# Optimization experiments

Hardware: AMD Instinct MI355X
Metric: run time of the kernel (lower is better)

## Reference

```python
import jax, jax.numpy as jnp
import numpy as np

ROPE_BASE = 10000.0
WINDOW = 1024  # per_layer_sliding_window
SCALE = 0.08838834764831845  # 1/sqrt(128)
NEG_INF = -1e30


def _apply_rope(x, positions):
    # x: [B, S, H, D]; positions: [B, S] int
    D = x.shape[-1]
    inv_freq = 1.0 / (ROPE_BASE ** (jnp.arange(0, D, 2, dtype=jnp.float32) / D))  # [D/2]
    ang = positions.astype(jnp.float32)[..., None] * inv_freq          # [B, S, D/2]
    cos = jnp.cos(ang)[:, :, None, :]                                   # [B, S, 1, D/2]
    sin = jnp.sin(ang)[:, :, None, :]
    x1, x2 = x[..., : D // 2], x[..., D // 2 :]
    return jnp.concatenate([x1 * cos - x2 * sin, x2 * cos + x1 * sin], axis=-1)


def setup_inputs() -> dict:
    key = jax.random.key(0)
    k1, k2, k3, k4 = jax.random.split(key, 4)
    B, S, H, KV, D = 1, 2048, 32, 8, 128
    q = jax.random.normal(k1, (B, S, H, D), dtype=jnp.float32)
    k = jax.random.normal(k2, (B, S, KV, D), dtype=jnp.float32)
    v = jax.random.normal(k3, (B, S, KV, D), dtype=jnp.float32)
    positions = jnp.broadcast_to(jnp.arange(S, dtype=jnp.int32), (B, S))
    sinks = jax.random.normal(k4, (H,), dtype=jnp.float32)
    return {"q": q, "k": k, "v": v, "positions": positions, "sinks": sinks}


def reference(q, k, v, positions, sinks):
    # q: [B,S,H,D]; k,v: [B,S,KV,D]; positions: [B,S]; sinks: [H]
    B, S, H, D = q.shape
    KV = k.shape[2]
    group = H // KV

    qr = _apply_rope(q, positions)
    kr = _apply_rope(k, positions)

    # GQA: expand kv heads to match q heads
    kr = jnp.repeat(kr, group, axis=2)  # [B,S,H,D]
    ve = jnp.repeat(v, group, axis=2)   # [B,S,H,D]

    scores = jnp.einsum("bqhd,bkhd->bhqk", qr, kr) * SCALE  # [B,H,Q,K]

    pq = positions[:, :, None]  # [B,Q,1]
    pk = positions[:, None, :]  # [B,1,K]
    allowed = (pk <= pq) & (pq - pk < WINDOW)               # causal + sliding window
    scores = jnp.where(allowed[:, None, :, :], scores, NEG_INF)

    # softmax with per-head attention sink logit in the denominator
    sink = sinks[None, :, None]                             # [1,H,1]
    m = jnp.maximum(jnp.max(scores, axis=-1), sink)         # [B,H,Q]
    p = jnp.exp(scores - m[..., None])                      # [B,H,Q,K]
    denom = jnp.sum(p, axis=-1) + jnp.exp(sink - m)         # [B,H,Q]
    out = jnp.einsum("bhqk,bkhd->bqhd", p, ve) / denom.transpose(0, 2, 1)[..., None]
    return out  # [B,S,H,D]
```

## Files before the change

### kernel.cpp

```cpp
#include <hip/hip_runtime.h>

#define S_LEN 2048
#define NH 32
#define NKV 8
#define HD 128
#define WINDOW 1024
#define NEG_INF_F -1e30f
#define NEG_L2_10K_O64 -0.2076205059304601f
#define LOG2E_F 1.442695040888963f

typedef unsigned short ushort_t;
typedef __attribute__((ext_vector_type(4))) short bf16x4;
typedef __attribute__((ext_vector_type(8))) short short8;
typedef __attribute__((ext_vector_type(2))) unsigned uint2v;
typedef __attribute__((ext_vector_type(4))) float floatx4;

static __device__ __forceinline__ float fexp2(float x) {
  return __builtin_amdgcn_exp2f(x);
}

static __device__ __forceinline__ ushort_t f2bf(float f) {
  union { float f; unsigned u; } un; un.f = f;
  unsigned r = un.u + 0x7fffu + ((un.u >> 16) & 1u);
  return (ushort_t)(r >> 16);
}

static __device__ __forceinline__ unsigned pack2bf(float a, float b) {
  return (unsigned)f2bf(a) | ((unsigned)f2bf(b) << 16);
}

static __device__ __forceinline__ unsigned packP(float a, float b) {
  unsigned ua = __builtin_bit_cast(unsigned, a) + 0x8000u;
  unsigned ub = __builtin_bit_cast(unsigned, b) + 0x8000u;
  return __builtin_amdgcn_perm(ub, ua, 0x07060302u);
}

__device__ __forceinline__ void gl_lds16(const ushort_t* g, ushort_t* l) {
  __builtin_amdgcn_global_load_lds(
      (const __attribute__((address_space(1))) unsigned int*)g,
      (__attribute__((address_space(3))) unsigned int*)l, 16, 0, 0);
}

__global__ __launch_bounds__(256) void prep_kv(
    const float* __restrict__ k, const float* __restrict__ v,
    const int* __restrict__ positions, ushort_t* __restrict__ Kr,
    ushort_t* __restrict__ Vt) {
  __shared__ float lv[64][129];
  const int kv = blockIdx.x & 7;
  const int s0 = (blockIdx.x >> 3) * 64;
  const int tid = threadIdx.x;
  {
    const int i = tid & 63;
    const int wrow = tid >> 6;
    const float invf = fexp2((float)i * NEG_L2_10K_O64);
#pragma unroll 4
    for (int it = 0; it < 16; ++it) {
      int s = s0 + it * 4 + wrow;
      float pos = (float)positions[s];
      const float* kp = k + ((size_t)s * NKV + kv) * HD;
      float x1 = kp[i], x2 = kp[i + 64];
      float sn, cs;
      __sincosf(pos * invf, &sn, &cs);
      ushort_t* o = Kr + ((size_t)kv * S_LEN + s) * HD;
      o[i] = f2bf(x1 * cs - x2 * sn);
      o[i + 64] = f2bf(x2 * cs + x1 * sn);
    }
  }
  {
    const int d = tid & 127;
    const int r2 = tid >> 7;
#pragma unroll
    for (int it = 0; it < 32; ++it) {
      int row = it * 2 + r2;
      lv[row][d] = v[((size_t)(s0 + row) * NKV + kv) * HD + d];
    }
  }
  __syncthreads();
  {
    unsigned* Vreg = (unsigned*)(Vt + ((size_t)(kv * 32 + (s0 >> 6)) * HD) * 64);
#pragma unroll
    for (int it = 0; it < 16; ++it) {
      int idx = it * 256 + tid;
      int d = idx >> 5, j = idx & 31;
      Vreg[idx] = pack2bf(lv[2 * j][d], lv[2 * j + 1][d]);
    }
  }
}

__global__ __launch_bounds__(256, 3) void attn_kernel(
    const float* __restrict__ q, const int* __restrict__ positions,
    const float* __restrict__ sinks, const ushort_t* __restrict__ Kr,
    const ushort_t* __restrict__ Vt, float* __restrict__ out) {
  __shared__ __align__(16) ushort_t smem[16384];
  __shared__ float lsx[64];

  const int tid = threadIdx.x;
  const int w = tid >> 6;
  const int lane = tid & 63;
  const int quad = lane >> 4;
  const int l16 = lane & 15;
  const int hp = w >> 1;
  const int kh = w & 1;
  const int kv = blockIdx.x & 7;
  const int bid = blockIdx.x >> 3;
  const int h0 = kv * 4 + hp * 2;
  const float QSCALE = (float)(0.08838834764831845 * 1.4426950408889634);

  const ushort_t* KrH = Kr + (size_t)kv * S_LEN * HD;
  const ushort_t* VtH = Vt + (size_t)kv * 32 * HD * 64;

  int tiles[2];
  int ntiles;
  if (bid < 64) { tiles[0] = bid + 64; tiles[1] = 0; ntiles = 1; }
  else          { tiles[0] = bid - 64; tiles[1] = 127 - bid; ntiles = 2; }

  int kgo0, kgo1, vgo0, vgo1;
  { int key = tid >> 4;          kgo0 = key * HD + (((tid & 15) ^ (key & 15)) * 8); }
  { int s2 = 256 + tid; int key = s2 >> 4;
                                 kgo1 = key * HD + (((s2 & 15) ^ (key & 15)) * 8); }
  { int n = tid;       vgo0 = (n >> 2) * 64 + (((n & 3) ^ ((n >> 4) & 3)) * 8); }
  { int n = 256 + tid; vgo1 = (n >> 2) * 64 + (((n & 3) ^ ((n >> 4) & 3)) * 8); }
  const int kdst0 = (tid & 192) * 8;
  const int kdst1 = (256 + (tid & 192)) * 8;
  const int vdst0 = 8192 + (tid & 192) * 8;
  const int vdst1 = 8192 + 2048 + (tid & 192) * 8;
  const int kb8 = kh * 2 + (quad >> 1);
  const int vrd = (l16 * 4 + (kb8 ^ (l16 >> 2))) * 8 + (quad & 1) * 4;

  auto stage = [&](int b, int koff) {
    const ushort_t* kb = KrH + (size_t)koff * HD;
    const ushort_t* vb = VtH + (size_t)(koff >> 6) * HD * 64 + (koff & 32);
    gl_lds16(kb + kgo0, smem + b * 4096 + kdst0);
    gl_lds16(kb + kgo1, smem + b * 4096 + kdst1);
    gl_lds16(vb + vgo0, smem + b * 4096 + vdst0);
    gl_lds16(vb + vgo1, smem + b * 4096 + vdst1);
  };

  for (int ti = 0; ti < ntiles; ++ti) {
    const int tile = tiles[ti];
    const int q0 = tile * 16;

    {
      const int hw = kv * 4 + w;
      ushort_t* Qsw = smem + w * 2048;
      const float invf = fexp2((float)lane * NEG_L2_10K_O64);
#pragma unroll 4
      for (int row = 0; row < 16; ++row) {
        float pos = (float)positions[q0 + row];
        const float* qp = q + ((size_t)(q0 + row) * NH + hw) * HD;
        float x1 = qp[lane], x2 = qp[lane + 64];
        float sn, cs;
        __sincosf(pos * invf, &sn, &cs);
        float o1 = (x1 * cs - x2 * sn) * QSCALE;
        float o2 = (x2 * cs + x1 * sn) * QSCALE;
        int c1_ = (lane >> 3) ^ row;
        int c2_ = ((lane >> 3) + 8) ^ row;
        Qsw[row * 128 + c1_ * 8 + (lane & 7)] = f2bf(o1);
        Qsw[row * 128 + c2_ * 8 + (lane & 7)] = f2bf(o2);
      }
    }
    __syncthreads();
    short8 qf0[4], qf1[4];
    {
      const ushort_t* Qr0 = smem + (hp * 2) * 2048;
      const ushort_t* Qr1 = smem + (hp * 2 + 1) * 2048;
#pragma unroll
      for (int t = 0; t < 4; ++t) {
        int off = l16 * 128 + (((4 * t + quad) ^ l16) * 8);
        qf0[t] = *(const short8*)&Qr0[off];
        qf1[t] = *(const short8*)&Qr1[off];
      }
    }
    __syncthreads();

    floatx4 OA[8], OB[8];
#pragma unroll
    for (int i = 0; i < 8; ++i) {
      OA[i] = (floatx4){0.f, 0.f, 0.f, 0.f};
      OB[i] = (floatx4){0.f, 0.f, 0.f, 0.f};
    }
    float lsumA = 0.f, lsumB = 0.f;

    const int cbeg = (q0 > 1023) ? ((q0 - 1023) >> 5) : 0;
    const int cend = (q0 + 15) >> 5;

    stage(0, cbeg * 32);
    __syncthreads();

    for (int ci = cbeg; ci <= cend; ++ci) {
      const int b = (ci - cbeg) & 1;
      const int koff = ci * 32;
      if (ci < cend) stage(b ^ 1, koff + 32);

      const ushort_t* KsB = smem + b * 4096 + (kh * 16) * 128;
      floatx4 sA = {0.f, 0.f, 0.f, 0.f}, sB = {0.f, 0.f, 0.f, 0.f};
#pragma unroll
      for (int t = 0; t < 4; ++t) {
        short8 kf = *(const short8*)&KsB[l16 * 128 + (((4 * t + quad) ^ l16) * 8)];
        sA = __builtin_amdgcn_mfma_f32_16x16x32_bf16(kf, qf0[t], sA, 0, 0, 0);
        sB = __builtin_amdgcn_mfma_f32_16x16x32_bf16(kf, qf1[t], sB, 0, 0, 0);
      }

      if (koff + 31 > q0 || koff < q0 - 1008) {
        const int qp_ = q0 + l16;
        const int kb_ = koff + kh * 16 + quad * 4;
#pragma unroll
        for (int r = 0; r < 4; ++r) {
          int ki = kb_ + r;
          bool ok = (ki <= qp_) && (qp_ - ki < WINDOW);
          if (!ok) { sA[r] = NEG_INF_F; sB[r] = NEG_INF_F; }
        }
      }

      float pA[4], pB[4];
#pragma unroll
      for (int r = 0; r < 4; ++r) { pA[r] = fexp2(sA[r]); pB[r] = fexp2(sB[r]); }
      lsumA += (pA[0] + pA[1]) + (pA[2] + pA[3]);
      lsumB += (pB[0] + pB[1]) + (pB[2] + pB[3]);

      uint2v ua, ub;
      ua[0] = packP(pA[0], pA[1]); ua[1] = packP(pA[2], pA[3]);
      ub[0] = packP(pB[0], pB[1]); ub[1] = packP(pB[2], pB[3]);
      bf16x4 pfA = __builtin_bit_cast(bf16x4, ua);
      bf16x4 pfB = __builtin_bit_cast(bf16x4, ub);

      const ushort_t* VsB = smem + 8192 + b * 4096;
#pragma unroll
      for (int dt = 0; dt < 8; ++dt) {
        bf16x4 vf = *(const bf16x4*)&VsB[vrd + dt * 512];
        OA[dt] = __builtin_amdgcn_mfma_f32_16x16x16bf16_1k(vf, pfA, OA[dt], 0, 0, 0);
        OB[dt] = __builtin_amdgcn_mfma_f32_16x16x16bf16_1k(vf, pfB, OB[dt], 0, 0, 0);
      }

      __syncthreads();
    }

    lsumA += __shfl_xor(lsumA, 16); lsumA += __shfl_xor(lsumA, 32);
    lsumB += __shfl_xor(lsumB, 16); lsumB += __shfl_xor(lsumB, 32);
    float* Lf = (float*)smem;
    const int lfb = lane * 4;
    float rlA = 0.f, rlB = 0.f;

    if (kh == 1 && quad == 0) {
      lsx[hp * 32 + l16] = lsumA;
      lsx[hp * 32 + 16 + l16] = lsumB;
    }
#pragma unroll
    for (int m = 0; m < 2; ++m) {
      if (kh == 1) {
#pragma unroll
        for (int t = 0; t < 4; ++t) {
          *(floatx4*)&Lf[((hp * 2 + 0) * 4 + t) * 256 + lfb] = OA[m * 4 + t];
          *(floatx4*)&Lf[((hp * 2 + 1) * 4 + t) * 256 + lfb] = OB[m * 4 + t];
        }
      }
      __syncthreads();
      if (kh == 0) {
        if (m == 0) {
          float denA = lsumA + lsx[hp * 32 + l16] + fexp2(sinks[h0] * LOG2E_F);
          float denB = lsumB + lsx[hp * 32 + 16 + l16] + fexp2(sinks[h0 + 1] * LOG2E_F);
          rlA = 1.0f / denA;
          rlB = 1.0f / denB;
        }
        float* opA = out + ((size_t)(q0 + l16) * NH + h0) * HD + quad * 4;
        float* opB = opA + HD;
#pragma unroll
        for (int t = 0; t < 4; ++t) {
          floatx4 pv = *(const floatx4*)&Lf[((hp * 2 + 0) * 4 + t) * 256 + lfb];
          floatx4 vv;
#pragma unroll
          for (int e = 0; e < 4; ++e) vv[e] = (OA[m * 4 + t][e] + pv[e]) * rlA;
          *(floatx4*)(opA + (m * 4 + t) * 16) = vv;
          pv = *(const floatx4*)&Lf[((hp * 2 + 1) * 4 + t) * 256 + lfb];
#pragma unroll
          for (int e = 0; e < 4; ++e) vv[e] = (OB[m * 4 + t][e] + pv[e]) * rlB;
          *(floatx4*)(opB + (m * 4 + t) * 16) = vv;
        }
      }
      __syncthreads();
    }
  }
}

extern "C" void kernel_launch(void* const* d_in, const int* in_sizes, int n_in,
                              void* d_out, int out_size, void* d_ws, size_t ws_size,
                              hipStream_t stream) {
  const float* q = (const float*)d_in[0];
  const float* k = (const float*)d_in[1];
  const float* v = (const float*)d_in[2];
  const int* positions = (const int*)d_in[3];
  const float* sinks = (const float*)d_in[4];
  float* out = (float*)d_out;

  ushort_t* Kr = (ushort_t*)d_ws;
  ushort_t* Vt = Kr + (size_t)NKV * S_LEN * HD;

  prep_kv<<<NKV * (S_LEN / 64), 256, 0, stream>>>(k, v, positions, Kr, Vt);
  attn_kernel<<<NKV * 96, 256, 0, stream>>>(q, positions, sinks, Kr, Vt, out);
}
```

Baseline: 137.5 us.

## Triple-buffer K/V tiles in LDS with prefetch distance two and partial vmcnt waits

```diff
diff --git a/kernel.cpp b/kernel.cpp
--- a/kernel.cpp
+++ b/kernel.cpp
@@ -91,7 +91,7 @@
     const float* __restrict__ q, const int* __restrict__ positions,
     const float* __restrict__ sinks, const ushort_t* __restrict__ Kr,
     const ushort_t* __restrict__ Vt, float* __restrict__ out) {
-  __shared__ __align__(16) ushort_t smem[16384];
+  __shared__ __align__(16) ushort_t smem[24576];
   __shared__ float lsx[64];
 
   const int tid = threadIdx.x;
@@ -122,18 +122,20 @@
   { int n = 256 + tid; vgo1 = (n >> 2) * 64 + (((n & 3) ^ ((n >> 4) & 3)) * 8); }
   const int kdst0 = (tid & 192) * 8;
   const int kdst1 = (256 + (tid & 192)) * 8;
-  const int vdst0 = 8192 + (tid & 192) * 8;
-  const int vdst1 = 8192 + 2048 + (tid & 192) * 8;
+  const int vdst0 = (tid & 192) * 8;
+  const int vdst1 = 2048 + (tid & 192) * 8;
   const int kb8 = kh * 2 + (quad >> 1);
   const int vrd = (l16 * 4 + (kb8 ^ (l16 >> 2))) * 8 + (quad & 1) * 4;
 
   auto stage = [&](int b, int koff) {
     const ushort_t* kb = KrH + (size_t)koff * HD;
     const ushort_t* vb = VtH + (size_t)(koff >> 6) * HD * 64 + (koff & 32);
-    gl_lds16(kb + kgo0, smem + b * 4096 + kdst0);
-    gl_lds16(kb + kgo1, smem + b * 4096 + kdst1);
-    gl_lds16(vb + vgo0, smem + b * 4096 + vdst0);
-    gl_lds16(vb + vgo1, smem + b * 4096 + vdst1);
+    ushort_t* Kb = smem + b * 4096;
+    ushort_t* Vb = smem + 12288 + b * 4096;
+    gl_lds16(kb + kgo0, Kb + kdst0);
+    gl_lds16(kb + kgo1, Kb + kdst1);
+    gl_lds16(vb + vgo0, Vb + vdst0);
+    gl_lds16(vb + vgo1, Vb + vdst1);
   };
 
   for (int ti = 0; ti < ntiles; ++ti) {
@@ -185,12 +187,22 @@
     const int cend = (q0 + 15) >> 5;
 
     stage(0, cbeg * 32);
-    __syncthreads();
-
+    if (cbeg < cend) {
+      stage(1, cbeg * 32 + 32);
+      asm volatile("s_waitcnt vmcnt(4)" ::: "memory");
+    } else {
+      asm volatile("s_waitcnt vmcnt(0)" ::: "memory");
+    }
+    __builtin_amdgcn_sched_barrier(0);
+    __builtin_amdgcn_s_barrier();
+
+    int b = 0;
     for (int ci = cbeg; ci <= cend; ++ci) {
-      const int b = (ci - cbeg) & 1;
       const int koff = ci * 32;
-      if (ci < cend) stage(b ^ 1, koff + 32);
+      if (ci + 2 <= cend) {
+        int bp2 = (b >= 1) ? (b - 1) : (b + 2);
+        stage(bp2, koff + 64);
+      }
 
       const ushort_t* KsB = smem + b * 4096 + (kh * 16) * 128;
       floatx4 sA = {0.f, 0.f, 0.f, 0.f}, sB = {0.f, 0.f, 0.f, 0.f};
@@ -224,7 +236,7 @@
       bf16x4 pfA = __builtin_bit_cast(bf16x4, ua);
       bf16x4 pfB = __builtin_bit_cast(bf16x4, ub);
 
-      const ushort_t* VsB = smem + 8192 + b * 4096;
+      const ushort_t* VsB = smem + 12288 + b * 4096;
 #pragma unroll
       for (int dt = 0; dt < 8; ++dt) {
         bf16x4 vf = *(const bf16x4*)&VsB[vrd + dt * 512];
@@ -232,8 +244,18 @@
         OB[dt] = __builtin_amdgcn_mfma_f32_16x16x16bf16_1k(vf, pfB, OB[dt], 0, 0, 0);
       }
 
-      __syncthreads();
-    }
+      if (ci + 2 <= cend) {
+        asm volatile("s_waitcnt vmcnt(4)" ::: "memory");
+        __builtin_amdgcn_sched_barrier(0);
+        __builtin_amdgcn_s_barrier();
+      } else if (ci + 1 <= cend) {
+        asm volatile("s_waitcnt vmcnt(0)" ::: "memory");
+        __builtin_amdgcn_sched_barrier(0);
+        __builtin_amdgcn_s_barrier();
+      }
+      b = (b + 1 == 3) ? 0 : b + 1;
+    }
+    __syncthreads();
 
     lsumA += __shfl_xor(lsumA, 16); lsumA += __shfl_xor(lsumA, 32);
     lsumB += __shfl_xor(lsumB, 16); lsumB += __shfl_xor(lsumB, 32);
```

After: 139.5 us. Within noise of the previous version (+1.4%).

## Load K/V MFMA fragments directly from global memory instead of LDS staging

Applied to the files above, without the earlier changes.

```diff
diff --git a/kernel.cpp b/kernel.cpp
--- a/kernel.cpp
+++ b/kernel.cpp
@@ -33,12 +33,6 @@
   unsigned ua = __builtin_bit_cast(unsigned, a) + 0x8000u;
   unsigned ub = __builtin_bit_cast(unsigned, b) + 0x8000u;
   return __builtin_amdgcn_perm(ub, ua, 0x07060302u);
-}
-
-__device__ __forceinline__ void gl_lds16(const ushort_t* g, ushort_t* l) {
-  __builtin_amdgcn_global_load_lds(
-      (const __attribute__((address_space(1))) unsigned int*)g,
-      (__attribute__((address_space(3))) unsigned int*)l, 16, 0, 0);
 }
 
 __global__ __launch_bounds__(256) void prep_kv(
@@ -91,7 +85,7 @@
     const float* __restrict__ q, const int* __restrict__ positions,
     const float* __restrict__ sinks, const ushort_t* __restrict__ Kr,
     const ushort_t* __restrict__ Vt, float* __restrict__ out) {
-  __shared__ __align__(16) ushort_t smem[16384];
+  __shared__ __align__(16) ushort_t smem[8192];
   __shared__ float lsx[64];
 
   const int tid = threadIdx.x;
@@ -114,27 +108,8 @@
   if (bid < 64) { tiles[0] = bid + 64; tiles[1] = 0; ntiles = 1; }
   else          { tiles[0] = bid - 64; tiles[1] = 127 - bid; ntiles = 2; }
 
-  int kgo0, kgo1, vgo0, vgo1;
-  { int key = tid >> 4;          kgo0 = key * HD + (((tid & 15) ^ (key & 15)) * 8); }
-  { int s2 = 256 + tid; int key = s2 >> 4;
-                                 kgo1 = key * HD + (((s2 & 15) ^ (key & 15)) * 8); }
-  { int n = tid;       vgo0 = (n >> 2) * 64 + (((n & 3) ^ ((n >> 4) & 3)) * 8); }
-  { int n = 256 + tid; vgo1 = (n >> 2) * 64 + (((n & 3) ^ ((n >> 4) & 3)) * 8); }
-  const int kdst0 = (tid & 192) * 8;
-  const int kdst1 = (256 + (tid & 192)) * 8;
-  const int vdst0 = 8192 + (tid & 192) * 8;
-  const int vdst1 = 8192 + 2048 + (tid & 192) * 8;
-  const int kb8 = kh * 2 + (quad >> 1);
-  const int vrd = (l16 * 4 + (kb8 ^ (l16 >> 2))) * 8 + (quad & 1) * 4;
-
-  auto stage = [&](int b, int koff) {
-    const ushort_t* kb = KrH + (size_t)koff * HD;
-    const ushort_t* vb = VtH + (size_t)(koff >> 6) * HD * 64 + (koff & 32);
-    gl_lds16(kb + kgo0, smem + b * 4096 + kdst0);
-    gl_lds16(kb + kgo1, smem + b * 4096 + kdst1);
-    gl_lds16(vb + vgo0, smem + b * 4096 + vdst0);
-    gl_lds16(vb + vgo1, smem + b * 4096 + vdst1);
-  };
+  const int kconst = (kh * 16 + l16) * HD + quad * 8;
+  const int vconst = l16 * 64 + kh * 16 + quad * 4;
 
   for (int ti = 0; ti < ntiles; ++ti) {
     const int tile = tiles[ti];
@@ -184,21 +159,23 @@
     const int cbeg = (q0 > 1023) ? ((q0 - 1023) >> 5) : 0;
     const int cend = (q0 + 15) >> 5;
 
-    stage(0, cbeg * 32);
-    __syncthreads();
-
     for (int ci = cbeg; ci <= cend; ++ci) {
-      const int b = (ci - cbeg) & 1;
       const int koff = ci * 32;
-      if (ci < cend) stage(b ^ 1, koff + 32);
-
-      const ushort_t* KsB = smem + b * 4096 + (kh * 16) * 128;
+      const ushort_t* kp = KrH + (size_t)koff * HD + kconst;
+      const ushort_t* vp = VtH + (size_t)(koff >> 6) * 8192 + (koff & 32) + vconst;
+
+      bf16x4 vf[8];
+#pragma unroll
+      for (int dt = 0; dt < 8; ++dt) vf[dt] = *(const bf16x4*)(vp + dt * 1024);
+      short8 kf[4];
+#pragma unroll
+      for (int t = 0; t < 4; ++t) kf[t] = *(const short8*)(kp + t * 32);
+
       floatx4 sA = {0.f, 0.f, 0.f, 0.f}, sB = {0.f, 0.f, 0.f, 0.f};
 #pragma unroll
       for (int t = 0; t < 4; ++t) {
-        short8 kf = *(const short8*)&KsB[l16 * 128 + (((4 * t + quad) ^ l16) * 8)];
-        sA = __builtin_amdgcn_mfma_f32_16x16x32_bf16(kf, qf0[t], sA, 0, 0, 0);
-        sB = __builtin_amdgcn_mfma_f32_16x16x32_bf16(kf, qf1[t], sB, 0, 0, 0);
+        sA = __builtin_amdgcn_mfma_f32_16x16x32_bf16(kf[t], qf0[t], sA, 0, 0, 0);
+        sB = __builtin_amdgcn_mfma_f32_16x16x32_bf16(kf[t], qf1[t], sB, 0, 0, 0);
       }
 
       if (koff + 31 > q0 || koff < q0 - 1008) {
@@ -224,16 +201,13 @@
       bf16x4 pfA = __builtin_bit_cast(bf16x4, ua);
       bf16x4 pfB = __builtin_bit_cast(bf16x4, ub);
 
-      const ushort_t* VsB = smem + 8192 + b * 4096;
 #pragma unroll
       for (int dt = 0; dt < 8; ++dt) {
-        bf16x4 vf = *(const bf16x4*)&VsB[vrd + dt * 512];
-        OA[dt] = __builtin_amdgcn_mfma_f32_16x16x16bf16_1k(vf, pfA, OA[dt], 0, 0, 0);
-        OB[dt] = __builtin_amdgcn_mfma_f32_16x16x16bf16_1k(vf, pfB, OB[dt], 0, 0, 0);
-      }
-
-      __syncthreads();
-    }
+        OA[dt] = __builtin_amdgcn_mfma_f32_16x16x16bf16_1k(vf[dt], pfA, OA[dt], 0, 0, 0);
+        OB[dt] = __builtin_amdgcn_mfma_f32_16x16x16bf16_1k(vf[dt], pfB, OB[dt], 0, 0, 0);
+      }
+    }
+    __syncthreads();
 
     lsumA += __shfl_xor(lsumA, 16); lsumA += __shfl_xor(lsumA, 32);
     lsumB += __shfl_xor(lsumB, 16); lsumB += __shfl_xor(lsumB, 32);
```

Result: slower. 231.5 us (+68.4%).
